# Kernel optimization log

Hardware: AMD Instinct MI355X
Metric: run time of the kernel (lower is better)

The kernel has to match this reference:

```python
import jax, jax.numpy as jnp
import numpy as np

LN_EPS = 1e-5

def _layernorm(x, g, b):
    mu = jnp.mean(x, axis=-1, keepdims=True)
    var = jnp.var(x, axis=-1, keepdims=True)
    return (x - mu) * jax.lax.rsqrt(var + LN_EPS) * g + b

def setup_inputs() -> dict:
    key = jax.random.key(0)
    ks = jax.random.split(key, 12)
    B, E, R = 32, 64, 36
    Dt, Di, D = 768, 2048, 512
    s = 0.02
    return {
        "text_feats": jax.random.normal(ks[0], (B, E, Dt), jnp.float32),
        "image_feats": jax.random.normal(ks[1], (B, R, Di), jnp.float32),
        "W_text": jax.random.normal(ks[2], (Dt, D), jnp.float32) * s,
        "b_text": jnp.zeros((D,), jnp.float32),
        "g_text": jnp.ones((D,), jnp.float32),
        "beta_text": jnp.zeros((D,), jnp.float32),
        "W_img": jax.random.normal(ks[3], (Di, D), jnp.float32) * s,
        "b_img": jnp.zeros((D,), jnp.float32),
        "g_img": jnp.ones((D,), jnp.float32),
        "beta_img": jnp.zeros((D,), jnp.float32),
        "W1": jax.random.normal(ks[4], (2 * D, D), jnp.float32) * s,
        "b1": jnp.zeros((D,), jnp.float32),
        "W2": jax.random.normal(ks[5], (D, 1), jnp.float32) * s,
        "b2": jnp.zeros((1,), jnp.float32),
    }

def reference(text_feats, image_feats, W_text, b_text, g_text, beta_text,
              W_img, b_img, g_img, beta_img, W1, b1, W2, b2):
    B, E, _ = text_feats.shape
    R = image_feats.shape[1]
    D = W_text.shape[1]
    # projections: Linear -> ReLU -> LayerNorm
    text_aligned = _layernorm(jax.nn.relu(text_feats @ W_text + b_text), g_text, beta_text)   # [B,E,D]
    image_aligned = _layernorm(jax.nn.relu(image_feats @ W_img + b_img), g_img, beta_img)     # [B,R,D]
    # pairwise scorer: split W1 to avoid materializing the [B,E,R,2D] concat
    W1_t, W1_i = W1[:D], W1[D:]
    h_t = text_aligned @ W1_t                 # [B,E,D]
    h_i = image_aligned @ W1_i + b1           # [B,R,D]
    h = jax.nn.relu(h_t[:, :, None, :] + h_i[:, None, :, :])  # [B,E,R,D]
    scores_raw = jnp.squeeze(h @ W2, -1) + b2[0]               # [B,E,R]
    alignment_scores = jax.nn.sigmoid(scores_raw)
    # softmax over flattened (E*R) per batch
    w = jax.nn.softmax(alignment_scores.reshape(B, E * R), axis=1).reshape(B, E, R)
    # weighted sum over regions, mean over entities
    aggregated = jnp.einsum('ber,brd->bd', w, image_aligned) / E   # [B,D]
    return alignment_scores, aggregated
```

## Files before the change

### kernel.cpp

```cpp
#include <hip/hip_runtime.h>
#include <math.h>

#define LN_EPS 1e-5f

typedef __attribute__((ext_vector_type(8))) short bf16x8;
typedef __attribute__((ext_vector_type(4))) float f32x4;
typedef unsigned short ushort_t;
typedef unsigned int uint_t;

__device__ __forceinline__ ushort_t f2bf(float f) {
    uint_t u = __float_as_uint(f);
    u += 0x7FFF + ((u >> 16) & 1);
    return (ushort_t)(u >> 16);
}

__global__ __launch_bounds__(256) void prep_kernel(
    const float* __restrict__ text, const float* __restrict__ image,
    ushort_t* __restrict__ text_bf, ushort_t* __restrict__ image_bf,
    const float* __restrict__ W_text, const float* __restrict__ W_img,
    const float* __restrict__ W1,
    const float* __restrict__ g_text, const float* __restrict__ beta_text,
    const float* __restrict__ g_img, const float* __restrict__ beta_img,
    ushort_t* __restrict__ Wt_t, ushort_t* __restrict__ Wi_t,
    ushort_t* __restrict__ W1t_g, ushort_t* __restrict__ W1i_g,
    float* __restrict__ stats, float* __restrict__ vparts)
{
    __shared__ float t[32][33];
    const int bid = blockIdx.x;
    const int tid = threadIdx.x;
    if (bid < 3840) {
        const int i4 = (bid * 256 + tid) * 4;
        const float* src; ushort_t* dst; int off;
        if (i4 < 1572864) { src = text;  dst = text_bf;  off = i4; }
        else              { src = image; dst = image_bf; off = i4 - 1572864; }
        float4 v = *(const float4*)(src + off);
        ushort4 o;
        o.x = f2bf(v.x); o.y = f2bf(v.y); o.z = f2bf(v.z); o.w = f2bf(v.w);
        *(ushort4*)(dst + off) = o;
        return;
    }
    int local = bid - 3840;
    if (local < 1920) {
        const float* src; ushort_t* dst; int K; const float* gs = nullptr;
        if      (local < 384)  { src = W_text;       dst = Wt_t;  K = 768;  }
        else if (local < 1408) { src = W_img;        dst = Wi_t;  K = 2048; local -= 384; }
        else if (local < 1664) { src = W1;           dst = W1t_g; K = 512;  local -= 1408; gs = g_text; }
        else                   { src = W1 + 512*512; dst = W1i_g; K = 512;  local -= 1664; gs = g_img; }
        const int ntk = K / 32;
        const int k0 = (local % ntk) * 32;
        const int n0 = (local / ntk) * 32;
        const int x = tid % 32, y = tid / 32;
        #pragma unroll
        for (int j = 0; j < 4; ++j)
            t[y + 8 * j][x] = src[(size_t)(k0 + y + 8 * j) * 512 + n0 + x];
        __syncthreads();
        const float gv = gs ? gs[k0 + x] : 1.f;
        #pragma unroll
        for (int j = 0; j < 4; ++j)
            dst[(size_t)(n0 + y + 8 * j) * K + k0 + x] = f2bf(t[x][y + 8 * j] * gv);
        return;
    }
    if (local == 1920) {
        for (int i = tid; i < 6400; i += 256) stats[i] = 0.f;
        return;
    }
    {
        const int j    = local - 1921;
        const int half = j >> 2;
        const int jj   = j & 3;
        const float* cg = half ? g_img : g_text;
        const float* cb = half ? beta_img : beta_text;
        const float* Wb = W1 + (size_t)(half * 512 + jj * 128) * 512;
        const int n = tid;
        float ag0 = 0.f, ab0 = 0.f, ag1 = 0.f, ab1 = 0.f;
        #pragma unroll 4
        for (int k = 0; k < 128; ++k) {
            const float c1 = cg[jj * 128 + k];
            const float c2 = cb[jj * 128 + k];
            const float w0 = Wb[(size_t)k * 512 + n];
            const float w1 = Wb[(size_t)k * 512 + n + 256];
            ag0 = fmaf(c1, w0, ag0); ab0 = fmaf(c2, w0, ab0);
            ag1 = fmaf(c1, w1, ag1); ab1 = fmaf(c2, w1, ab1);
        }
        float* vg = vparts + (size_t)(half * 2 + 0) * 2048 + jj * 512;
        float* vb = vparts + (size_t)(half * 2 + 1) * 2048 + jj * 512;
        vg[n] = ag0; vg[n + 256] = ag1;
        vb[n] = ab0; vb[n + 256] = ab1;
    }
}

__device__ __forceinline__ void gemm_core(
    const ushort_t* __restrict__ A, const ushort_t* __restrict__ Bt, int K,
    int brow, int bcol, int wave, int lane, float (&red)[4][64][64])
{
    const int q  = lane >> 4;
    const int mj = lane & 15;
    const ushort_t* Ab = A  + (size_t)(brow + mj) * K + q * 8;
    const ushort_t* Bb = Bt + (size_t)(bcol + mj) * K + q * 8;
    const int kw0    = wave * (K >> 2);
    const int ksteps = K >> 7;

    f32x4 acc[4][4] = {};
    #pragma unroll 2
    for (int s = 0; s < ksteps; ++s) {
        const int k = kw0 + s * 32;
        bf16x8 af[4], bf[4];
        #pragma unroll
        for (int i = 0; i < 4; ++i) {
            af[i] = *(const bf16x8*)(Ab + (size_t)i * 16 * K + k);
            bf[i] = *(const bf16x8*)(Bb + (size_t)i * 16 * K + k);
        }
        #pragma unroll
        for (int mi = 0; mi < 4; ++mi)
            #pragma unroll
            for (int ni = 0; ni < 4; ++ni)
                acc[mi][ni] = __builtin_amdgcn_mfma_f32_16x16x32_bf16(
                    af[mi], bf[ni], acc[mi][ni], 0, 0, 0);
    }
    #pragma unroll
    for (int mi = 0; mi < 4; ++mi)
        #pragma unroll
        for (int ni = 0; ni < 4; ++ni)
            #pragma unroll
            for (int r = 0; r < 4; ++r)
                red[wave][mi * 16 + q * 4 + r][ni * 16 + mj] = acc[mi][ni][r];
    __syncthreads();
}

__global__ __launch_bounds__(256) void gemm1_kernel(
    const ushort_t* __restrict__ A0, const ushort_t* __restrict__ B0,
    const float* __restrict__ bias0, ushort_t* __restrict__ Cb0,
    float* __restrict__ Cf0, float* __restrict__ st0, int K0,
    const ushort_t* __restrict__ A1, const ushort_t* __restrict__ B1,
    const float* __restrict__ bias1, ushort_t* __restrict__ Cb1,
    float* __restrict__ Cf1, float* __restrict__ st1, int K1,
    int ysplit)
{
    __shared__ float red[4][64][64];
    const ushort_t* A; const ushort_t* Bt; const float* bias;
    ushort_t* Cb; float* Cf; float* st; int K;
    int yy = blockIdx.y;
    if (yy < ysplit) { A=A0; Bt=B0; bias=bias0; Cb=Cb0; Cf=Cf0; st=st0; K=K0; }
    else { A=A1; Bt=B1; bias=bias1; Cb=Cb1; Cf=Cf1; st=st1; K=K1; yy -= ysplit; }

    const int tid  = threadIdx.x;
    const int brow = yy * 64;
    const int bcol = blockIdx.x * 64;
    gemm_core(A, Bt, K, brow, bcol, tid >> 6, tid & 63, red);

    #pragma unroll
    for (int g = 0; g < 4; ++g) {
        const int idx = g * 1024 + tid * 4;
        const int row = idx >> 6, col = idx & 63;
        float4 v0 = *(float4*)&red[0][row][col];
        float4 v1 = *(float4*)&red[1][row][col];
        float4 v2 = *(float4*)&red[2][row][col];
        float4 v3 = *(float4*)&red[3][row][col];
        float4 o;
        o.x = (v0.x + v1.x) + (v2.x + v3.x);
        o.y = (v0.y + v1.y) + (v2.y + v3.y);
        o.z = (v0.z + v1.z) + (v2.z + v3.z);
        o.w = (v0.w + v1.w) + (v2.w + v3.w);
        float4 bv = *(const float4*)&bias[bcol + col];
        o.x = fmaxf(o.x + bv.x, 0.f); o.y = fmaxf(o.y + bv.y, 0.f);
        o.z = fmaxf(o.z + bv.z, 0.f); o.w = fmaxf(o.w + bv.w, 0.f);
        ushort4 ob;
        ob.x = f2bf(o.x); ob.y = f2bf(o.y); ob.z = f2bf(o.z); ob.w = f2bf(o.w);
        *(ushort4*)&Cb[(size_t)(brow + row) * 512 + bcol + col] = ob;
        if (Cf) *(float4*)&Cf[(size_t)(brow + row) * 512 + bcol + col] = o;
        float s1 = (o.x + o.y) + (o.z + o.w);
        float s2 = fmaf(o.x, o.x, fmaf(o.y, o.y, fmaf(o.z, o.z, o.w * o.w)));
        #pragma unroll
        for (int off = 8; off; off >>= 1) {
            s1 += __shfl_down(s1, off, 16);
            s2 += __shfl_down(s2, off, 16);
        }
        if ((tid & 15) == 0) {
            atomicAdd(&st[(size_t)(brow + row) * 2],     s1);
            atomicAdd(&st[(size_t)(brow + row) * 2 + 1], s2);
        }
    }
}

__global__ __launch_bounds__(256) void gemm2_kernel(
    const ushort_t* __restrict__ A0, const ushort_t* __restrict__ B0,
    const float* __restrict__ bias0, float* __restrict__ C0,
    const float* __restrict__ st0, const float* __restrict__ gW0,
    const float* __restrict__ bW0, int K0,
    const ushort_t* __restrict__ A1, const ushort_t* __restrict__ B1,
    const float* __restrict__ bias1, float* __restrict__ C1,
    const float* __restrict__ st1, const float* __restrict__ gW1,
    const float* __restrict__ bW1, int K1,
    int ysplit)
{
    __shared__ float red[4][64][64];
    const ushort_t* A; const ushort_t* Bt; const float* bias; float* C;
    const float* st; const float* gW; const float* bW; int K;
    int yy = blockIdx.y;
    if (yy < ysplit) { A=A0; Bt=B0; bias=bias0; C=C0; st=st0; gW=gW0; bW=bW0; K=K0; }
    else { A=A1; Bt=B1; bias=bias1; C=C1; st=st1; gW=gW1; bW=bW1; K=K1; yy -= ysplit; }

    const int tid  = threadIdx.x;
    const int brow = yy * 64;
    const int bcol = blockIdx.x * 64;
    gemm_core(A, Bt, K, brow, bcol, tid >> 6, tid & 63, red);

    #pragma unroll
    for (int g = 0; g < 4; ++g) {
        const int idx = g * 1024 + tid * 4;
        const int row = idx >> 6, col = idx & 63;
        float4 v0 = *(float4*)&red[0][row][col];
        float4 v1 = *(float4*)&red[1][row][col];
        float4 v2 = *(float4*)&red[2][row][col];
        float4 v3 = *(float4*)&red[3][row][col];
        float4 s;
        s.x = (v0.x + v1.x) + (v2.x + v3.x);
        s.y = (v0.y + v1.y) + (v2.y + v3.y);
        s.z = (v0.z + v1.z) + (v2.z + v3.z);
        s.w = (v0.w + v1.w) + (v2.w + v3.w);
        const float st1v = st[(size_t)(brow + row) * 2];
        const float st2v = st[(size_t)(brow + row) * 2 + 1];
        const float mu   = st1v * (1.f / 512.f);
        const float var  = st2v * (1.f / 512.f) - mu * mu;
        const float rstd = rsqrtf(var + LN_EPS);
        const int c = bcol + col;
        float4 gw = *(const float4*)&gW[c];
        float4 bw = *(const float4*)&bW[c];
        #pragma unroll
        for (int j = 1; j < 4; ++j) {
            float4 gp = *(const float4*)&gW[j * 512 + c];
            float4 bp = *(const float4*)&bW[j * 512 + c];
            gw.x += gp.x; gw.y += gp.y; gw.z += gp.z; gw.w += gp.w;
            bw.x += bp.x; bw.y += bp.y; bw.z += bp.z; bw.w += bp.w;
        }
        const float rm = rstd * mu;
        float4 o;
        o.x = fmaf(rstd, s.x, fmaf(-rm, gw.x, bw.x));
        o.y = fmaf(rstd, s.y, fmaf(-rm, gw.y, bw.y));
        o.z = fmaf(rstd, s.z, fmaf(-rm, gw.z, bw.z));
        o.w = fmaf(rstd, s.w, fmaf(-rm, gw.w, bw.w));
        if (bias) {
            float4 bb = *(const float4*)&bias[c];
            o.x += bb.x; o.y += bb.y; o.z += bb.z; o.w += bb.w;
        }
        *(float4*)&C[(size_t)(brow + row) * 512 + c] = o;
    }
}

__global__ __launch_bounds__(256) void scores_kernel(
    const float* __restrict__ ht, const float* __restrict__ hi,
    const float* __restrict__ W2, const float* __restrict__ b2,
    float* __restrict__ scores)
{
    const int be   = blockIdx.x;
    const int b    = be >> 6;
    const int tid  = threadIdx.x;
    const int lane = tid & 63;
    const int wave = tid >> 6;

    float htv[8], w2v[8];
    const float* htp = ht + (size_t)be * 512;
    #pragma unroll
    for (int j = 0; j < 8; ++j) {
        htv[j] = htp[lane + 64 * j];
        w2v[j] = W2[lane + 64 * j];
    }
    const float bb = b2[0];
    const float* hib = hi + (size_t)b * 36 * 512;

    for (int r = wave; r < 36; r += 4) {
        const float* hir = hib + (size_t)r * 512;
        float acc = 0.f;
        #pragma unroll
        for (int j = 0; j < 8; ++j) {
            float h = fmaxf(htv[j] + hir[lane + 64 * j], 0.f);
            acc = fmaf(h, w2v[j], acc);
        }
        #pragma unroll
        for (int off = 32; off; off >>= 1) acc += __shfl_down(acc, off);
        if (lane == 0) {
            float sr = acc + bb;
            scores[(size_t)be * 36 + r] = 1.f / (1.f + expf(-sr));
        }
    }
}

__global__ __launch_bounds__(256) void agg_kernel(
    const float* __restrict__ scores, const float* __restrict__ img,
    const float* __restrict__ stats, const float* __restrict__ g_img,
    const float* __restrict__ beta_img, float* __restrict__ outAgg)
{
    const int b   = blockIdx.x;
    const int tid = threadIdx.x;
    const float* sc = scores + (size_t)b * 2304;

    __shared__ float part[4][36];
    __shared__ float sexp[36];
    __shared__ float inv_s;
    __shared__ float coef[36], cmu[36];

    const int e4 = tid >> 6;
    const int r  = tid & 63;
    if (r < 36) {
        float p = 0.f;
        #pragma unroll
        for (int e = 0; e < 16; ++e) p += expf(sc[(e * 4 + e4) * 36 + r]);
        part[e4][r] = p;
    }
    __syncthreads();
    if (tid < 36) sexp[tid] = part[0][tid] + part[1][tid] + part[2][tid] + part[3][tid];
    __syncthreads();
    if (tid < 64) {
        float v = (tid < 36) ? sexp[tid] : 0.f;
        #pragma unroll
        for (int off = 32; off; off >>= 1) v += __shfl_down(v, off);
        if (tid == 0) inv_s = 1.f / (v * 64.f);
    }
    __syncthreads();
    const float inv = inv_s;
    if (tid < 36) {
        const float s1 = stats[(size_t)(b * 36 + tid) * 2];
        const float s2 = stats[(size_t)(b * 36 + tid) * 2 + 1];
        const float mu   = s1 * (1.f / 512.f);
        const float var  = s2 * (1.f / 512.f) - mu * mu;
        const float rstd = rsqrtf(var + LN_EPS);
        const float c = sexp[tid] * inv * rstd;
        coef[tid] = c;
        cmu[tid]  = c * mu;
    }
    __syncthreads();
    float S1 = 0.f;
    #pragma unroll
    for (int rr = 0; rr < 36; ++rr) S1 += cmu[rr];
    const float S0 = 1.f / 64.f;

    const float* ib = img + (size_t)b * 36 * 512;
    for (int d = tid; d < 512; d += 256) {
        float acc = 0.f;
        #pragma unroll
        for (int rr = 0; rr < 36; ++rr)
            acc = fmaf(coef[rr], ib[rr * 512 + d], acc);
        outAgg[(size_t)b * 512 + d] = fmaf(g_img[d], acc - S1, beta_img[d] * S0);
    }
}

extern "C" void kernel_launch(void* const* d_in, const int* in_sizes, int n_in,
                              void* d_out, int out_size, void* d_ws, size_t ws_size,
                              hipStream_t stream)
{
    const float* text      = (const float*)d_in[0];
    const float* image     = (const float*)d_in[1];
    const float* W_text    = (const float*)d_in[2];
    const float* b_text    = (const float*)d_in[3];
    const float* g_text    = (const float*)d_in[4];
    const float* beta_text = (const float*)d_in[5];
    const float* W_img     = (const float*)d_in[6];
    const float* b_img     = (const float*)d_in[7];
    const float* g_img     = (const float*)d_in[8];
    const float* beta_img  = (const float*)d_in[9];
    const float* W1        = (const float*)d_in[10];
    const float* b1        = (const float*)d_in[11];
    const float* W2        = (const float*)d_in[12];
    const float* b2        = (const float*)d_in[13];

    float* out_scores = (float*)d_out;
    float* out_agg    = (float*)d_out + 73728;

    char* ws = (char*)d_ws;
    ushort_t* ta_bf    = (ushort_t*)(ws);
    ushort_t* ia_bf    = (ushort_t*)(ws + 2097152);
    float*    ia       = (float*)(ws + 3276800);
    float*    ht       = (float*)(ws + 5636096);
    float*    hi       = (float*)(ws + 9830400);
    ushort_t* text_bf  = (ushort_t*)(ws + 12189696);
    ushort_t* image_bf = (ushort_t*)(ws + 15335424);
    ushort_t* Wt_t     = (ushort_t*)(ws + 20054016);
    ushort_t* Wi_t     = (ushort_t*)(ws + 20840448);
    ushort_t* W1t_g    = (ushort_t*)(ws + 22937600);
    ushort_t* W1i_g    = (ushort_t*)(ws + 23461888);
    float*    stats    = (float*)(ws + 23986176);
    float*    vparts   = (float*)(ws + 24011776);

    prep_kernel<<<5769, 256, 0, stream>>>(
        text, image, text_bf, image_bf, W_text, W_img, W1,
        g_text, beta_text, g_img, beta_img,
        Wt_t, Wi_t, W1t_g, W1i_g, stats, vparts);
    gemm1_kernel<<<dim3(8, 50), 256, 0, stream>>>(
        text_bf, Wt_t, b_text, ta_bf, nullptr, stats, 768,
        image_bf, Wi_t, b_img, ia_bf, ia, stats + 4096, 2048,
        32);
    gemm2_kernel<<<dim3(8, 50), 256, 0, stream>>>(
        ta_bf, W1t_g, nullptr, ht, stats,        vparts,        vparts + 2048, 512,
        ia_bf, W1i_g, b1,      hi, stats + 4096, vparts + 4096, vparts + 6144, 512,
        32);
    scores_kernel<<<2048, 256, 0, stream>>>(ht, hi, W2, b2, out_scores);
    agg_kernel<<<32, 256, 0, stream>>>(out_scores, ia, stats + 4096,
                                       g_img, beta_img, out_agg);
}
```

Baseline: 154.1 us.

## Fuse aggregation into scores kernel via per-batch last-block counter

Merges the separate aggregation kernel into the scores kernel. The last block to finish for each batch, detected with an atomic counter that the prep kernel zeroes, computes the softmax-weighted aggregation. This removes one kernel launch and the serial tail of a 32-block kernel. The gemm1 problem order is also swapped so the larger image GEMM runs first, with the split row count changed from 32 to 18 to rebalance tile assignment. The cost is atomics, extra thread fences, and some extra shared memory in every scores block.

```diff
diff --git a/kernel.cpp b/kernel.cpp
--- a/kernel.cpp
+++ b/kernel.cpp
@@ -23,7 +23,8 @@
     const float* __restrict__ g_img, const float* __restrict__ beta_img,
     ushort_t* __restrict__ Wt_t, ushort_t* __restrict__ Wi_t,
     ushort_t* __restrict__ W1t_g, ushort_t* __restrict__ W1i_g,
-    float* __restrict__ stats, float* __restrict__ vparts)
+    float* __restrict__ stats, float* __restrict__ vparts,
+    uint_t* __restrict__ cnt)
 {
     __shared__ float t[32][33];
     const int bid = blockIdx.x;
@@ -62,6 +63,7 @@
     }
     if (local == 1920) {
         for (int i = tid; i < 6400; i += 256) stats[i] = 0.f;
+        if (tid < 32) cnt[tid] = 0u;
         return;
     }
     {
@@ -247,10 +249,13 @@
     }
 }
 
-__global__ __launch_bounds__(256) void scores_kernel(
+__global__ __launch_bounds__(256) void scores_agg_kernel(
     const float* __restrict__ ht, const float* __restrict__ hi,
     const float* __restrict__ W2, const float* __restrict__ b2,
-    float* __restrict__ scores)
+    float* __restrict__ scores,
+    const float* __restrict__ img, const float* __restrict__ stats,
+    const float* __restrict__ g_img, const float* __restrict__ beta_img,
+    float* __restrict__ outAgg, uint_t* __restrict__ cnt)
 {
     const int be   = blockIdx.x;
     const int b    = be >> 6;
@@ -283,22 +288,24 @@
             scores[(size_t)be * 36 + r] = 1.f / (1.f + expf(-sr));
         }
     }
-}
-
-__global__ __launch_bounds__(256) void agg_kernel(
-    const float* __restrict__ scores, const float* __restrict__ img,
-    const float* __restrict__ stats, const float* __restrict__ g_img,
-    const float* __restrict__ beta_img, float* __restrict__ outAgg)
-{
-    const int b   = blockIdx.x;
-    const int tid = threadIdx.x;
-    const float* sc = scores + (size_t)b * 2304;
+
+    __shared__ uint_t done;
+    __syncthreads();
+    if (tid == 0) {
+        __threadfence();
+        done = atomicAdd(&cnt[b], 1u);
+    }
+    __syncthreads();
+    if (done != 63u) return;
+    if (tid == 0) __threadfence();
+    __syncthreads();
 
     __shared__ float part[4][36];
     __shared__ float sexp[36];
     __shared__ float inv_s;
     __shared__ float coef[36], cmu[36];
 
+    const float* sc = scores + (size_t)b * 2304;
     const int e4 = tid >> 6;
     const int r  = tid & 63;
     if (r < 36) {
@@ -380,20 +387,21 @@
     ushort_t* W1i_g    = (ushort_t*)(ws + 23461888);
     float*    stats    = (float*)(ws + 23986176);
     float*    vparts   = (float*)(ws + 24011776);
+    uint_t*   cnt      = (uint_t*)(ws + 24044544);
 
     prep_kernel<<<5769, 256, 0, stream>>>(
         text, image, text_bf, image_bf, W_text, W_img, W1,
         g_text, beta_text, g_img, beta_img,
-        Wt_t, Wi_t, W1t_g, W1i_g, stats, vparts);
+        Wt_t, Wi_t, W1t_g, W1i_g, stats, vparts, cnt);
     gemm1_kernel<<<dim3(8, 50), 256, 0, stream>>>(
+        image_bf, Wi_t, b_img, ia_bf, ia, stats + 4096, 2048,
         text_bf, Wt_t, b_text, ta_bf, nullptr, stats, 768,
-        image_bf, Wi_t, b_img, ia_bf, ia, stats + 4096, 2048,
-        32);
+        18);
     gemm2_kernel<<<dim3(8, 50), 256, 0, stream>>>(
         ta_bf, W1t_g, nullptr, ht, stats,        vparts,        vparts + 2048, 512,
         ia_bf, W1i_g, b1,      hi, stats + 4096, vparts + 4096, vparts + 6144, 512,
         32);
-    scores_kernel<<<2048, 256, 0, stream>>>(ht, hi, W2, b2, out_scores);
-    agg_kernel<<<32, 256, 0, stream>>>(out_scores, ia, stats + 4096,
-                                       g_img, beta_img, out_agg);
-}
+    scores_agg_kernel<<<2048, 256, 0, stream>>>(
+        ht, hi, W2, b2, out_scores,
+        ia, stats + 4096, g_img, beta_img, out_agg, cnt);
+}
```

After: 203.9 us. 32.3% more time.
